# Performance work log

Measured on AMD Instinct MI355X. Metric: run time of the kernel, lower is better.

## Reference

```python
import jax, jax.numpy as jnp
import numpy as np

B, C, T = 16, 48, 96
PATCH, TOPK, ALPHA = 12, 3, 0.5
FF = 64  # 2 ** ceil(log2(C))
EPS = 1e-5


def setup_inputs() -> dict:
    key = jax.random.key(0)
    ks = jax.random.split(key, 12)
    n = lambda k, s, sc=0.05: jax.random.normal(k, s, jnp.float32) * sc
    return {
        "x": jax.random.normal(ks[0], (B, C, T), jnp.float32),
        # BatchNorm affine params (training-mode BN: batch statistics)
        "g0": 1.0 + n(ks[1], (C * T,)), "b0": n(ks[2], (C * T,)),
        "g1": 1.0 + n(ks[3], (PATCH * C,)), "b1": n(ks[4], (PATCH * C,)),
        "g2": 1.0 + n(ks[5], (PATCH * C,)), "b2": n(ks[6], (PATCH * C,)),
        # agg: Linear(patch, patch)
        "Wagg": n(ks[7], (PATCH, PATCH), 0.2), "bagg": jnp.zeros((PATCH,), jnp.float32),
        # sim_mlp: Linear(2, FF) -> GELU -> Linear(FF, 1)
        "W1": n(ks[8], (FF, 2), 0.5), "bm1": jnp.zeros((FF,), jnp.float32),
        "W2": n(ks[9], (1, FF), 0.2), "bm2": jnp.zeros((1,), jnp.float32),
        # msg_linear: Linear(1, 1)
        "wmsg": 1.0 + n(ks[10], (1, 1)), "bmsg": n(ks[11], (1,)),
    }


def _bn(x2, g, b):
    # training-mode BatchNorm1d: biased variance over the batch axis
    mu = jnp.mean(x2, axis=0)
    var = jnp.mean((x2 - mu) ** 2, axis=0)
    return (x2 - mu) * jax.lax.rsqrt(var + EPS) * g + b


def _forward(x, g0, b0, g1, b1, g2, b2, Wagg, bagg, W1, bm1, W2, bm2, wmsg, bmsg):
    gelu = lambda v: jax.nn.gelu(v, approximate=False)
    xn = _bn(x.reshape(B, -1), g0, b0).reshape(B, C, T)
    first = xn[:, :, :PATCH]                       # history window, copied through
    steps = (T - PATCH) // PATCH
    xs = xn[:, :, PATCH:].reshape(B, C, steps, PATCH).transpose(2, 0, 1, 3)  # [S,B,C,P]

    def step(prev, xw):
        inp = _bn(prev.reshape(B, -1), g1, b1).reshape(B, C, PATCH)
        inp = gelu(jnp.einsum('bcp,qp->bcq', inp, Wagg) + bagg)  # agg over time window
        res = inp + xw                                            # [B,C,P]
        t = _bn(res.reshape(B, -1), g2, b2).reshape(B, C, PATCH)
        t = jnp.transpose(t, (0, 2, 1))                           # [B,P,C]
        zi = jnp.broadcast_to(t[:, :, :, None], (B, PATCH, C, C))
        zj = jnp.broadcast_to(t[:, :, None, :], (B, PATCH, C, C))
        pair = jnp.stack([zi, zj], axis=-1)                       # [B,P,C,C,2]
        h = gelu(jnp.einsum('bpijk,fk->bpijf', pair, W1) + bm1)
        e = jnp.einsum('bpijf,of->bpijo', h, W2)[..., 0] + bm2[0]  # [B,P,C,C]
        _, idx = jax.lax.top_k(e, TOPK)                            # [B,P,C,k]
        mask = (jnp.arange(C)[None, None, None, None, :] == idx[..., None]).any(axis=-2)
        e = jnp.where(mask, e, -1e9)
        a = jax.nn.softmax(e, axis=-1)                             # [B,P,C,C]
        msg = t * wmsg[0, 0] + bmsg[0]                             # [B,P,C]
        znew = jnp.einsum('bpij,bpj->bpi', a, msg)
        out = res + ALPHA * jnp.transpose(znew, (0, 2, 1))         # [B,C,P]
        return out, out

    _, outs = jax.lax.scan(step, first, xs)                        # [S,B,C,P]
    rest = jnp.transpose(outs, (1, 2, 0, 3)).reshape(B, C, T - PATCH)
    return jnp.concatenate([first, rest], axis=-1)


def reference(x, g0, b0, g1, b1, g2, b2, Wagg, bagg, W1, bm1, W2, bm2, wmsg, bmsg):
    return _forward(x, g0, b0, g1, b1, g2, b2, Wagg, bagg, W1, bm1, W2, bm2, wmsg, bmsg)
```

## Files before the change

kernel.cpp:

```cpp
#include <hip/hip_runtime.h>
#include <math.h>

#define NB 16
#define NC 48
#define NT 96
#define NP 12
#define NFF 64
#define CT 4608
#define STEPS 7

__device__ __forceinline__ float erf_fast(float x) {
    float a = fabsf(x);
    float t = __builtin_amdgcn_rcpf(fmaf(0.3275911f, a, 1.0f));
    float p = t * fmaf(t, fmaf(t, fmaf(t, fmaf(t, 1.061405429f, -1.453152027f),
                                       1.421413741f), -0.284496736f), 0.254829592f);
    float E = __builtin_amdgcn_exp2f(-a * a * 1.4426950408889634f);
    float y = fmaf(-p, E, 1.0f);
    return copysignf(y, x);
}
__device__ __forceinline__ float gelu_exact(float u) {
    float e  = erf_fast(u * 0.70710678118654752f);
    float hu = 0.5f * u;
    return fmaf(hu, e, hu);
}

__global__ __launch_bounds__(256) void bn0_kernel(
    const float* __restrict__ x, const float* __restrict__ g0,
    const float* __restrict__ b0, float* __restrict__ xn, float* __restrict__ out)
{
    int f = blockIdx.x * blockDim.x + threadIdx.x;
    if (f >= CT) return;
    float v[NB];
    float s = 0.f;
#pragma unroll
    for (int b = 0; b < NB; b++) { v[b] = x[b * CT + f]; s += v[b]; }
    float mu = s * (1.f / NB);
    float var = 0.f;
#pragma unroll
    for (int b = 0; b < NB; b++) { float d = v[b] - mu; var = fmaf(d, d, var); }
    var *= (1.f / NB);
    float rs = rsqrtf(var + 1e-5f);
    float g = g0[f], bb = b0[f];
    int c = f / NT, tt = f % NT;
#pragma unroll
    for (int b = 0; b < NB; b++) {
        float y = (v[b] - mu) * rs * g + bb;
        xn[b * CT + f] = y;
        if (tt < NP) out[(b * NC + c) * NT + tt] = y;
    }
}

__global__ __launch_bounds__(192) void phase1_kernel(
    const float* __restrict__ prev_base,
    const float* __restrict__ xn,
    const float* __restrict__ g1, const float* __restrict__ b1,
    const float* __restrict__ g2, const float* __restrict__ b2,
    const float* __restrict__ Wagg, const float* __restrict__ bagg,
    float* __restrict__ res_ws, float* __restrict__ t_ws, int s)
{
    int c = blockIdx.x;
    int tid = threadIdx.x;
    int b = tid / NP, p = tid % NP;
    __shared__ float sh[192], shB[192], wagg[144];
    if (tid < 144) wagg[tid] = Wagg[tid];
    float v = prev_base[(b * NC + c) * NT + NP * s + p];
    sh[tid] = v;
    __syncthreads();
    float s1 = 0.f;
#pragma unroll
    for (int bb2 = 0; bb2 < NB; bb2++) s1 += sh[bb2 * NP + p];
    float mu = s1 * (1.f / NB);
    float var = 0.f;
#pragma unroll
    for (int bb2 = 0; bb2 < NB; bb2++) { float d = sh[bb2 * NP + p] - mu; var = fmaf(d, d, var); }
    var *= (1.f / NB);
    float inp = (v - mu) * rsqrtf(var + 1e-5f) * g1[c * NP + p] + b1[c * NP + p];
    shB[tid] = inp;
    __syncthreads();
    float acc = bagg[p];
#pragma unroll
    for (int pp = 0; pp < NP; pp++) acc = fmaf(shB[b * NP + pp], wagg[p * NP + pp], acc);
    float res = gelu_exact(acc) + xn[(b * NC + c) * NT + NP + NP * s + p];
    res_ws[(b * NC + c) * NP + p] = res;
    sh[tid] = res;
    __syncthreads();
    float s2 = 0.f;
#pragma unroll
    for (int bb2 = 0; bb2 < NB; bb2++) s2 += sh[bb2 * NP + p];
    float mu2 = s2 * (1.f / NB);
    float var2 = 0.f;
#pragma unroll
    for (int bb2 = 0; bb2 < NB; bb2++) { float d = sh[bb2 * NP + p] - mu2; var2 = fmaf(d, d, var2); }
    var2 *= (1.f / NB);
    float t = (res - mu2) * rsqrtf(var2 + 1e-5f) * g2[c * NP + p] + b2[c * NP + p];
    t_ws[(b * NP + p) * NC + c] = t;
}

__global__ __launch_bounds__(192) void edge_kernel(
    const float* __restrict__ t_ws, const float* __restrict__ res_ws,
    const float* __restrict__ W1, const float* __restrict__ bm1,
    const float* __restrict__ W2, const float* __restrict__ wmsg,
    const float* __restrict__ bmsg, float* __restrict__ out, int s)
{
    int tid = threadIdx.x;
    int row0 = blockIdx.x * 4;
    int bp = row0 / NC;
    int b = bp / NP, p = bp % NP;
    int i0 = row0 % NC;

    __shared__ float4 coef[NFF];
    __shared__ float tv[NC];
    __shared__ float erow[4][NC];
    __shared__ float red[4][2];

    if (tid < NFF) coef[tid] = make_float4(W1[2 * tid], W1[2 * tid + 1], bm1[tid], W2[tid]);
    if (tid < NC)  tv[tid] = t_ws[bp * NC + tid];
    if (tid < 8)   ((float*)red)[tid] = 0.f;
    __syncthreads();

    int rl = tid / NC, j = tid % NC;
    int i = i0 + rl;
    float zi = tv[i], zj = tv[j];

    float e = 0.f;
#pragma unroll 8
    for (int f = 0; f < NFF; f++) {
        float4 cf = coef[f];
        float u = fmaf(cf.x, zi, fmaf(cf.y, zj, cf.z));
        e = fmaf(gelu_exact(u), cf.w, e);
    }
    erow[rl][j] = e;
    __syncthreads();

    float mx = -1e30f;
    int rank = 0;
#pragma unroll 8
    for (int k = 0; k < NC; k++) {
        float ek = erow[rl][k];
        mx = fmaxf(mx, ek);
        rank += (ek > e) || (ek == e && k < j);
    }
    if (rank < 3) {
        float w = __builtin_amdgcn_exp2f((e - mx) * 1.4426950408889634f);
        float msg = fmaf(zj, wmsg[0], bmsg[0]);
        atomicAdd(&red[rl][0], w);
        atomicAdd(&red[rl][1], w * msg);
    }
    __syncthreads();

    if (j == 0) {
        float znew = red[rl][1] / red[rl][0];
        out[(b * NC + i) * NT + NP * (s + 1) + p] =
            res_ws[(b * NC + i) * NP + p] + 0.5f * znew;
    }
}

extern "C" void kernel_launch(void* const* d_in, const int* in_sizes, int n_in,
                              void* d_out, int out_size, void* d_ws, size_t ws_size,
                              hipStream_t stream)
{
    const float* x    = (const float*)d_in[0];
    const float* g0   = (const float*)d_in[1];
    const float* b0   = (const float*)d_in[2];
    const float* g1   = (const float*)d_in[3];
    const float* b1   = (const float*)d_in[4];
    const float* g2   = (const float*)d_in[5];
    const float* b2   = (const float*)d_in[6];
    const float* Wagg = (const float*)d_in[7];
    const float* bagg = (const float*)d_in[8];
    const float* W1   = (const float*)d_in[9];
    const float* bm1  = (const float*)d_in[10];
    const float* W2   = (const float*)d_in[11];
    const float* wmsg = (const float*)d_in[13];
    const float* bmsg = (const float*)d_in[14];
    float* out = (float*)d_out;

    float* xn     = (float*)d_ws;
    float* t_ws   = xn + (NB * CT);
    float* res_ws = t_ws + (NB * NP * NC);

    bn0_kernel<<<CT / 256, 256, 0, stream>>>(x, g0, b0, xn, out);
    for (int s = 0; s < STEPS; s++) {
        phase1_kernel<<<NC, 192, 0, stream>>>(out, xn, g1, b1, g2, b2, Wagg, bagg,
                                              res_ws, t_ws, s);
        edge_kernel<<<(NB * NP * NC) / 4, 192, 0, stream>>>(t_ws, res_ws, W1, bm1, W2,
                                                            wmsg, bmsg, out, s);
    }
}
```

Measured before the change: 228.4 us.

## Fuse all steps into one persistent kernel with software grid barriers

Replaces the BN0 kernel and the 14 per-step phase1/edge launches with a single persistent kernel of 576 blocks that synchronise through an atomic-counter grid barrier. Each block redundantly recomputes the phase-1 batchnorm/aggregation for its (b,p) pair from a shared-memory copy of the previous window. The edge stage now handles 16 rows per block with 4 rows per thread, and a top-3 prefilter skips most rank computations. This removes launch overhead and intermediate workspace traffic, but it relies on all 576 blocks being co-resident, otherwise the barrier deadlocks, and it duplicates the phase-1 work across blocks.

Result: slower. 659.4 us (+188.7%).

```diff
diff --git a/kernel.cpp b/kernel.cpp
--- a/kernel.cpp
+++ b/kernel.cpp
@@ -8,6 +8,8 @@
 #define NFF 64
 #define CT 4608
 #define STEPS 7
+#define NBLK 576
+#define NTHR 192
 
 __device__ __forceinline__ float erf_fast(float x) {
     float a = fabsf(x);
@@ -24,134 +26,219 @@
     return fmaf(hu, e, hu);
 }
 
-__global__ __launch_bounds__(256) void bn0_kernel(
-    const float* __restrict__ x, const float* __restrict__ g0,
-    const float* __restrict__ b0, float* __restrict__ xn, float* __restrict__ out)
-{
-    int f = blockIdx.x * blockDim.x + threadIdx.x;
-    if (f >= CT) return;
-    float v[NB];
-    float s = 0.f;
-#pragma unroll
-    for (int b = 0; b < NB; b++) { v[b] = x[b * CT + f]; s += v[b]; }
-    float mu = s * (1.f / NB);
-    float var = 0.f;
-#pragma unroll
-    for (int b = 0; b < NB; b++) { float d = v[b] - mu; var = fmaf(d, d, var); }
-    var *= (1.f / NB);
-    float rs = rsqrtf(var + 1e-5f);
-    float g = g0[f], bb = b0[f];
-    int c = f / NT, tt = f % NT;
-#pragma unroll
-    for (int b = 0; b < NB; b++) {
-        float y = (v[b] - mu) * rs * g + bb;
-        xn[b * CT + f] = y;
-        if (tt < NP) out[(b * NC + c) * NT + tt] = y;
+__device__ __forceinline__ void grid_barrier(unsigned* cnt, unsigned* gen) {
+    __syncthreads();
+    if (threadIdx.x == 0) {
+        __threadfence();
+        unsigned g = __hip_atomic_load(gen, __ATOMIC_RELAXED, __HIP_MEMORY_SCOPE_AGENT);
+        unsigned old = __hip_atomic_fetch_add(cnt, 1u, __ATOMIC_ACQ_REL, __HIP_MEMORY_SCOPE_AGENT);
+        if (old == NBLK - 1u) {
+            __hip_atomic_store(cnt, 0u, __ATOMIC_RELAXED, __HIP_MEMORY_SCOPE_AGENT);
+            __hip_atomic_fetch_add(gen, 1u, __ATOMIC_RELEASE, __HIP_MEMORY_SCOPE_AGENT);
+        } else {
+            while (__hip_atomic_load(gen, __ATOMIC_RELAXED, __HIP_MEMORY_SCOPE_AGENT) == g)
+                __builtin_amdgcn_s_sleep(2);
+        }
+        __threadfence();
     }
-}
-
-__global__ __launch_bounds__(192) void phase1_kernel(
-    const float* __restrict__ prev_base,
-    const float* __restrict__ xn,
+    __syncthreads();
+}
+
+__global__ __launch_bounds__(NTHR, 3) void fused_kernel(
+    const float* __restrict__ x,
+    const float* __restrict__ g0, const float* __restrict__ b0,
     const float* __restrict__ g1, const float* __restrict__ b1,
     const float* __restrict__ g2, const float* __restrict__ b2,
     const float* __restrict__ Wagg, const float* __restrict__ bagg,
-    float* __restrict__ res_ws, float* __restrict__ t_ws, int s)
-{
-    int c = blockIdx.x;
-    int tid = threadIdx.x;
-    int b = tid / NP, p = tid % NP;
-    __shared__ float sh[192], shB[192], wagg[144];
-    if (tid < 144) wagg[tid] = Wagg[tid];
-    float v = prev_base[(b * NC + c) * NT + NP * s + p];
-    sh[tid] = v;
-    __syncthreads();
-    float s1 = 0.f;
-#pragma unroll
-    for (int bb2 = 0; bb2 < NB; bb2++) s1 += sh[bb2 * NP + p];
-    float mu = s1 * (1.f / NB);
-    float var = 0.f;
-#pragma unroll
-    for (int bb2 = 0; bb2 < NB; bb2++) { float d = sh[bb2 * NP + p] - mu; var = fmaf(d, d, var); }
-    var *= (1.f / NB);
-    float inp = (v - mu) * rsqrtf(var + 1e-5f) * g1[c * NP + p] + b1[c * NP + p];
-    shB[tid] = inp;
-    __syncthreads();
-    float acc = bagg[p];
-#pragma unroll
-    for (int pp = 0; pp < NP; pp++) acc = fmaf(shB[b * NP + pp], wagg[p * NP + pp], acc);
-    float res = gelu_exact(acc) + xn[(b * NC + c) * NT + NP + NP * s + p];
-    res_ws[(b * NC + c) * NP + p] = res;
-    sh[tid] = res;
-    __syncthreads();
-    float s2 = 0.f;
-#pragma unroll
-    for (int bb2 = 0; bb2 < NB; bb2++) s2 += sh[bb2 * NP + p];
-    float mu2 = s2 * (1.f / NB);
-    float var2 = 0.f;
-#pragma unroll
-    for (int bb2 = 0; bb2 < NB; bb2++) { float d = sh[bb2 * NP + p] - mu2; var2 = fmaf(d, d, var2); }
-    var2 *= (1.f / NB);
-    float t = (res - mu2) * rsqrtf(var2 + 1e-5f) * g2[c * NP + p] + b2[c * NP + p];
-    t_ws[(b * NP + p) * NC + c] = t;
-}
-
-__global__ __launch_bounds__(192) void edge_kernel(
-    const float* __restrict__ t_ws, const float* __restrict__ res_ws,
     const float* __restrict__ W1, const float* __restrict__ bm1,
     const float* __restrict__ W2, const float* __restrict__ wmsg,
-    const float* __restrict__ bmsg, float* __restrict__ out, int s)
+    const float* __restrict__ bmsg,
+    float* __restrict__ out, float* __restrict__ xn, unsigned* __restrict__ bar)
 {
-    int tid = threadIdx.x;
-    int row0 = blockIdx.x * 4;
-    int bp = row0 / NC;
-    int b = bp / NP, p = bp % NP;
-    int i0 = row0 % NC;
-
+    const int blk = blockIdx.x, tid = threadIdx.x;
+
+    __shared__ float prev_sh[NB * NC * NP];
+    __shared__ float Aw[NC * NP];
+    __shared__ float bw[NC * NP];
+    __shared__ float bconst[NC];
+    __shared__ float res_sh[NB * NC];
+    __shared__ float tv[NC];
+    __shared__ float erow[16][49];
+    __shared__ float rowm1[16], rowm3[16];
+    __shared__ float red[16][2];
     __shared__ float4 coef[NFF];
-    __shared__ float tv[NC];
-    __shared__ float erow[4][NC];
-    __shared__ float red[4][2];
-
-    if (tid < NFF) coef[tid] = make_float4(W1[2 * tid], W1[2 * tid + 1], bm1[tid], W2[tid]);
-    if (tid < NC)  tv[tid] = t_ws[bp * NC + tid];
-    if (tid < 8)   ((float*)red)[tid] = 0.f;
-    __syncthreads();
-
-    int rl = tid / NC, j = tid % NC;
-    int i = i0 + rl;
-    float zi = tv[i], zj = tv[j];
-
-    float e = 0.f;
+    __shared__ float wgs[NP];
+
+    const int bp = blk / 3;
+    const int i0 = (blk % 3) * 16;
+    const int b = bp / NP, p = bp % NP;
+
+    if (tid < NFF)
+        coef[tid] = make_float4(W1[2 * tid], W1[2 * tid + 1], bm1[tid], W2[tid]);
+    if (tid < NP) wgs[tid] = Wagg[p * NP + tid];
+
+    if (blk < CT / NTHR) {
+        int f = blk * NTHR + tid;
+        float v[NB];
+        float s = 0.f;
+#pragma unroll
+        for (int bb = 0; bb < NB; bb++) { v[bb] = x[bb * CT + f]; s += v[bb]; }
+        float mu = s * (1.f / NB);
+        float var = 0.f;
+#pragma unroll
+        for (int bb = 0; bb < NB; bb++) { float d = v[bb] - mu; var = fmaf(d, d, var); }
+        var *= (1.f / NB);
+        float rs = rsqrtf(var + 1e-5f);
+        float g = g0[f], bbv = b0[f];
+        int c = f / NT, tt = f % NT;
+#pragma unroll
+        for (int bb = 0; bb < NB; bb++) {
+            float y = (v[bb] - mu) * rs * g + bbv;
+            xn[bb * CT + f] = y;
+            if (tt < NP) out[(bb * NC + c) * NT + tt] = y;
+        }
+    }
+    grid_barrier(bar, bar + 1);
+
+    const float wm = wmsg[0], bmv = bmsg[0], baggp = bagg[p];
+
+    for (int s = 0; s < STEPS; s++) {
+#pragma unroll
+        for (int it = 0; it < 12; it++) {
+            int idx = it * NTHR + tid;
+            int row = idx / 3, q = idx - row * 3;
+            *(float4*)&prev_sh[idx * 4] =
+                *(const float4*)&out[row * NT + NP * s + 4 * q];
+        }
+        __syncthreads();
+
+#pragma unroll
+        for (int u = 0; u < 3; u++) {
+            int f = tid + NTHR * u;
+            float sum = 0.f;
+#pragma unroll
+            for (int bb = 0; bb < NB; bb++) sum += prev_sh[bb * 576 + f];
+            float mu = sum * (1.f / NB);
+            float var = 0.f;
+#pragma unroll
+            for (int bb = 0; bb < NB; bb++) {
+                float d = prev_sh[bb * 576 + f] - mu; var = fmaf(d, d, var);
+            }
+            var *= (1.f / NB);
+            float rs = rsqrtf(var + 1e-5f);
+            float alpha = g1[f] * rs;
+            float beta  = fmaf(-mu, alpha, b1[f]);
+            float w = wgs[f % NP];
+            Aw[f] = alpha * w;
+            bw[f] = beta * w;
+        }
+        __syncthreads();
+        if (tid < NC) {
+            float acc = baggp;
+#pragma unroll
+            for (int q = 0; q < NP; q++) acc += bw[tid * NP + q];
+            bconst[tid] = acc;
+        }
+        __syncthreads();
+
+#pragma unroll
+        for (int u = 0; u < 4; u++) {
+            int o = tid + NTHR * u;
+            int c = o % NC;
+            float acc = bconst[c];
+            const float4* pv = (const float4*)&prev_sh[o * NP];
+            const float4* aw = (const float4*)&Aw[c * NP];
+#pragma unroll
+            for (int q = 0; q < 3; q++) {
+                float4 a4 = pv[q], w4 = aw[q];
+                acc = fmaf(a4.x, w4.x, acc); acc = fmaf(a4.y, w4.y, acc);
+                acc = fmaf(a4.z, w4.z, acc); acc = fmaf(a4.w, w4.w, acc);
+            }
+            res_sh[o] = gelu_exact(acc) + xn[o * NT + NP + NP * s + p];
+        }
+        __syncthreads();
+
+        if (tid < 32) ((float*)red)[tid] = 0.f;
+        if (tid < NC) {
+            int c = tid;
+            float sum = 0.f;
+#pragma unroll
+            for (int bb = 0; bb < NB; bb++) sum += res_sh[bb * NC + c];
+            float mu = sum * (1.f / NB);
+            float var = 0.f;
+#pragma unroll
+            for (int bb = 0; bb < NB; bb++) {
+                float d = res_sh[bb * NC + c] - mu; var = fmaf(d, d, var);
+            }
+            var *= (1.f / NB);
+            float rs = rsqrtf(var + 1e-5f);
+            tv[c] = (res_sh[b * NC + c] - mu) * rs * g2[c * NP + p] + b2[c * NP + p];
+        }
+        __syncthreads();
+
+        {
+            int j = tid % NC, rg = tid / NC;
+            float zj = tv[j];
+            float zi[4], e[4];
+#pragma unroll
+            for (int k = 0; k < 4; k++) { zi[k] = tv[i0 + rg + 4 * k]; e[k] = 0.f; }
+
+#pragma unroll 4
+            for (int f = 0; f < NFF; f++) {
+                float4 cf = coef[f];
+                float base = fmaf(cf.y, zj, cf.z);
+#pragma unroll
+                for (int k = 0; k < 4; k++) {
+                    float u = fmaf(cf.x, zi[k], base);
+                    e[k] = fmaf(gelu_exact(u), cf.w, e[k]);
+                }
+            }
+#pragma unroll
+            for (int k = 0; k < 4; k++) erow[rg + 4 * k][j] = e[k];
+            __syncthreads();
+
+            if (tid < 16) {
+                float m1 = -1e30f, m2 = -1e30f, m3 = -1e30f;
 #pragma unroll 8
-    for (int f = 0; f < NFF; f++) {
-        float4 cf = coef[f];
-        float u = fmaf(cf.x, zi, fmaf(cf.y, zj, cf.z));
-        e = fmaf(gelu_exact(u), cf.w, e);
-    }
-    erow[rl][j] = e;
-    __syncthreads();
-
-    float mx = -1e30f;
-    int rank = 0;
-#pragma unroll 8
-    for (int k = 0; k < NC; k++) {
-        float ek = erow[rl][k];
-        mx = fmaxf(mx, ek);
-        rank += (ek > e) || (ek == e && k < j);
-    }
-    if (rank < 3) {
-        float w = __builtin_amdgcn_exp2f((e - mx) * 1.4426950408889634f);
-        float msg = fmaf(zj, wmsg[0], bmsg[0]);
-        atomicAdd(&red[rl][0], w);
-        atomicAdd(&red[rl][1], w * msg);
-    }
-    __syncthreads();
-
-    if (j == 0) {
-        float znew = red[rl][1] / red[rl][0];
-        out[(b * NC + i) * NT + NP * (s + 1) + p] =
-            res_ws[(b * NC + i) * NP + p] + 0.5f * znew;
+                for (int k = 0; k < NC; k++) {
+                    float v = erow[tid][k];
+                    float n1 = fmaxf(m1, v), r1 = fminf(m1, v);
+                    float n2 = fmaxf(m2, r1), r2 = fminf(m2, r1);
+                    float n3 = fmaxf(m3, r2);
+                    m1 = n1; m2 = n2; m3 = n3;
+                }
+                rowm1[tid] = m1; rowm3[tid] = m3;
+            }
+            __syncthreads();
+
+            float msg = fmaf(zj, wm, bmv);
+#pragma unroll
+            for (int k = 0; k < 4; k++) {
+                int r = rg + 4 * k;
+                float ek = e[k];
+                if (ek >= rowm3[r]) {
+                    int rank = 0;
+                    for (int kk = 0; kk < NC; kk++) {
+                        float v = erow[r][kk];
+                        rank += (v > ek) || (v == ek && kk < j);
+                    }
+                    if (rank < 3) {
+                        float w = __builtin_amdgcn_exp2f((ek - rowm1[r]) * 1.4426950408889634f);
+                        atomicAdd(&red[r][0], w);
+                        atomicAdd(&red[r][1], w * msg);
+                    }
+                }
+            }
+            __syncthreads();
+
+            if (tid < 16) {
+                int i = i0 + tid;
+                float znew = red[tid][1] / red[tid][0];
+                out[(b * NC + i) * NT + NP * (s + 1) + p] =
+                    res_sh[b * NC + i] + 0.5f * znew;
+            }
+        }
+        if (s < STEPS - 1) grid_barrier(bar, bar + 1);
     }
 }
 
@@ -175,15 +262,11 @@
     const float* bmsg = (const float*)d_in[14];
     float* out = (float*)d_out;
 
-    float* xn     = (float*)d_ws;
-    float* t_ws   = xn + (NB * CT);
-    float* res_ws = t_ws + (NB * NP * NC);
-
-    bn0_kernel<<<CT / 256, 256, 0, stream>>>(x, g0, b0, xn, out);
-    for (int s = 0; s < STEPS; s++) {
-        phase1_kernel<<<NC, 192, 0, stream>>>(out, xn, g1, b1, g2, b2, Wagg, bagg,
-                                              res_ws, t_ws, s);
-        edge_kernel<<<(NB * NP * NC) / 4, 192, 0, stream>>>(t_ws, res_ws, W1, bm1, W2,
-                                                            wmsg, bmsg, out, s);
-    }
-}
+    float* xn = (float*)d_ws;
+    unsigned* bar = (unsigned*)((char*)d_ws + 73728 * 4);
+
+    hipMemsetAsync(bar, 0, 256, stream);
+    fused_kernel<<<NBLK, NTHR, 0, stream>>>(x, g0, b0, g1, b1, g2, b2, Wagg,
+                                            bagg, W1, bm1, W2, wmsg, bmsg,
+                                            out, xn, bar);
+}
```
